# Kernel tuning notes

Hardware: AMD Instinct MI355X
Metric: run time of the kernel (lower is better)

The kernel has to match this reference:

```python
import jax, jax.numpy as jnp
import numpy as np

B, S, D, H = 128, 512, 256, 256


def _lstm_cell(Wih, Whh, b, x_t, h, c):
    # PyTorch LSTM gate order: i, f, g, o. b = b_ih + b_hh (mathematically equivalent).
    z = x_t @ Wih.T + h @ Whh.T + b  # [B, 4H]
    i, f, g, o = jnp.split(z, 4, axis=-1)
    i = jax.nn.sigmoid(i)
    f = jax.nn.sigmoid(f)
    g = jnp.tanh(g)
    o = jax.nn.sigmoid(o)
    c = f * c + i * g
    h = o * jnp.tanh(c)
    return h, c


def setup_inputs() -> dict:
    key = jax.random.key(0)
    ks = jax.random.split(key, 12)
    s = 1.0 / np.sqrt(H)
    f32 = jnp.float32
    return {
        "x": jax.random.normal(ks[0], (B, S, D), f32),
        "enc_Wih": jax.random.uniform(ks[1], (4 * H, D), f32, -s, s),
        "enc_Whh": jax.random.uniform(ks[2], (4 * H, H), f32, -s, s),
        "enc_b": jax.random.uniform(ks[3], (4 * H,), f32, -s, s),
        "dec_Wih": jax.random.uniform(ks[4], (4 * H, D), f32, -s, s),
        "dec_Whh": jax.random.uniform(ks[5], (4 * H, H), f32, -s, s),
        "dec_b": jax.random.uniform(ks[6], (4 * H,), f32, -s, s),
        "W1_w": jax.random.uniform(ks[7], (H, H), f32, -s, s),
        "W1_b": jax.random.uniform(ks[8], (H,), f32, -s, s),
        "W2_w": jax.random.uniform(ks[9], (H, H), f32, -s, s),
        "W2_b": jax.random.uniform(ks[10], (H,), f32, -s, s),
        "vt_w": jax.random.uniform(ks[11], (H,), f32, -s, s),
    }


def reference(x, enc_Wih, enc_Whh, enc_b, dec_Wih, dec_Whh, dec_b,
              W1_w, W1_b, W2_w, W2_b, vt_w):
    b_, s_, d_ = x.shape
    h0 = jnp.zeros((b_, H), x.dtype)
    c0 = jnp.zeros((b_, H), x.dtype)

    # ---- encoder LSTM over time ----
    def enc_step(carry, x_t):
        h, c = carry
        h, c = _lstm_cell(enc_Wih, enc_Whh, enc_b, x_t, h, c)
        return (h, c), h

    (h, c), enc_out = jax.lax.scan(enc_step, (h0, c0), jnp.swapaxes(x, 0, 1))
    enc_out = jnp.swapaxes(enc_out, 0, 1)  # [B, S, H]

    # W1(encoder_outputs) is loop-invariant; compute once (same math as original)
    enc_proj = enc_out @ W1_w.T + W1_b  # [B, S, H]

    # ---- pointer decode loop ----
    def dec_step(carry, _):
        h, c, din = carry
        h, c = _lstm_cell(dec_Wih, dec_Whh, dec_b, din, h, c)
        q = h @ W2_w.T + W2_b  # [B, H]
        u = jnp.einsum('bsh,h->bs', jnp.tanh(enc_proj + q[:, None, :]), vt_w)
        probs = jax.nn.softmax(u, axis=1)  # [B, S]
        din = jnp.einsum('bs,bsh->bh', probs, enc_out)
        return (h, c, din), probs

    din0 = jnp.zeros((b_, d_), x.dtype)
    _, probs_seq = jax.lax.scan(dec_step, (h, c, din0), None, length=s_)
    return jnp.swapaxes(probs_seq, 0, 1)  # [B, S, S]
```

## Files before the change

### kernel.cpp

```cpp
#include <hip/hip_runtime.h>
#include <hip/hip_fp16.h>

typedef _Float16 h2_t __attribute__((ext_vector_type(2)));
typedef unsigned int u32x4 __attribute__((ext_vector_type(4)));

#define KEXP 2.8853900817779268f

#define BARRIER() do { \
    asm volatile("s_waitcnt lgkmcnt(0)" ::: "memory"); \
    __builtin_amdgcn_s_barrier(); \
    asm volatile("" ::: "memory"); \
} while (0)

__device__ __forceinline__ float fdot2(unsigned int a, unsigned int b, float c) {
#if __has_builtin(__builtin_amdgcn_fdot2)
    return __builtin_amdgcn_fdot2(__builtin_bit_cast(h2_t, a), __builtin_bit_cast(h2_t, b), c, false);
#else
    h2_t ha = __builtin_bit_cast(h2_t, a), hb = __builtin_bit_cast(h2_t, b);
    return c + (float)ha[0]*(float)hb[0] + (float)ha[1]*(float)hb[1];
#endif
}

__device__ __forceinline__ unsigned int pk16(float a, float b) {
    auto h = __builtin_amdgcn_cvt_pkrtz(a, b);
    return __builtin_bit_cast(unsigned int, h);
}

__device__ __forceinline__ float rcp_(float x) {
#if __has_builtin(__builtin_amdgcn_rcpf)
    return __builtin_amdgcn_rcpf(x);
#else
    return 1.0f / x;
#endif
}

__device__ __forceinline__ float sigm(float x) { return rcp_(1.0f + __expf(-x)); }
__device__ __forceinline__ float tanh_(float x) {
    float e = __expf(2.0f * x);
    return 1.0f - 2.0f * rcp_(e + 1.0f);
}

__device__ __forceinline__ unsigned int rcp1p2exp(unsigned int s) {
    __half2 e = h2exp2(__builtin_bit_cast(__half2, s));
    __half2 d = __hadd2(e, __float2half2_rn(1.0f));
    return __builtin_bit_cast(unsigned int, h2rcp(d));
}
__device__ __forceinline__ unsigned int hadd2u(unsigned int a, unsigned int b) {
    return __builtin_bit_cast(unsigned int,
        __hadd2(__builtin_bit_cast(__half2, a), __builtin_bit_cast(__half2, b)));
}

__device__ __forceinline__ void st_u32(unsigned int* p, unsigned int v) {
    __hip_atomic_store(p, v, __ATOMIC_RELAXED, __HIP_MEMORY_SCOPE_AGENT);
}
__device__ __forceinline__ unsigned int ld_u32(const unsigned int* p) {
    return __hip_atomic_load(p, __ATOMIC_RELAXED, __HIP_MEMORY_SCOPE_AGENT);
}
__device__ __forceinline__ float h2f_lo(unsigned int v) {
    return __half2float(__ushort_as_half((unsigned short)(v & 0xffffu)));
}
__device__ __forceinline__ float h2f_hi(unsigned int v) {
    return __half2float(__ushort_as_half((unsigned short)(v >> 16)));
}

__device__ __forceinline__ void pair_sync(unsigned int* flags, int fo_me, int fo_pr,
                                          unsigned int target, int t) {
    BARRIER();
    if (t == 0) {
        st_u32(&flags[fo_me], target);
        while (ld_u32(&flags[fo_pr]) < target) __builtin_amdgcn_s_sleep(1);
    }
    BARRIER();
}

__global__ void init_flags_kernel(unsigned int* flags) {
    flags[threadIdx.x * 32] = 0u;
}

__global__ __launch_bounds__(256) void prep_kernel(
    const float* __restrict__ encWhh, const float* __restrict__ decWih,
    const float* __restrict__ decWhh, const float* __restrict__ W2w,
    u32x4* __restrict__ We8, u32x4* __restrict__ Wi8, u32x4* __restrict__ Wh8, u32x4* __restrict__ W28)
{
    int id = blockIdx.x * 256 + threadIdx.x;
    if (id < 3 * 32768) {
        int mat = id >> 15, local = id & 32767;
        int j = local & 1023, k8 = local >> 10;
        const float* src = mat == 0 ? encWhh : (mat == 1 ? decWih : decWhh);
        u32x4* dst = mat == 0 ? We8 : (mat == 1 ? Wi8 : Wh8);
        const float* p = src + (size_t)j * 256 + k8 * 8;
        float4 a = *(const float4*)p; float4 c = *(const float4*)(p + 4);
        u32x4 v; v[0] = pk16(a.x, a.y); v[1] = pk16(a.z, a.w);
        v[2] = pk16(c.x, c.y); v[3] = pk16(c.z, c.w);
        dst[k8 * 1024 + j] = v;
    } else {
        int local = id - 3 * 32768;
        if (local < 8192) {
            int m = local & 255, k8 = local >> 8;
            const float* p = W2w + (size_t)m * 256 + k8 * 8;
            float4 a = *(const float4*)p; float4 c = *(const float4*)(p + 4);
            u32x4 v; v[0] = pk16(a.x, a.y); v[1] = pk16(a.z, a.w);
            v[2] = pk16(c.x, c.y); v[3] = pk16(c.z, c.w);
            W28[k8 * 256 + m] = v;
        }
    }
}

template<int A_IS_F16, int TR_OUT>
__global__ __launch_bounds__(256) void gemm_kernel(
    const void* __restrict__ A_, const float* __restrict__ Bw,
    const float* __restrict__ bias, unsigned short* __restrict__ C, int N, float scale)
{
    __shared__ float As[16][68];
    __shared__ float Bs[16][132];
    const int t = threadIdx.x;
    const int row0 = blockIdx.y * 64, col0 = blockIdx.x * 128;
    const int ty = t >> 4, tx = t & 15;
    const int lm = t & 63, lkq = t >> 6;
    const int ln = t & 127, lkq2 = t >> 7;
    float acc[4][8] = {};
    for (int k0 = 0; k0 < 256; k0 += 16) {
        float4 av;
        if constexpr (A_IS_F16) {
            const unsigned short* A = (const unsigned short*)A_;
            uint2 ha = *(const uint2*)(A + (size_t)(row0 + lm) * 256 + k0 + lkq * 4);
            h2_t h0 = __builtin_bit_cast(h2_t, ha.x);
            h2_t h1 = __builtin_bit_cast(h2_t, ha.y);
            av = make_float4((float)h0[0], (float)h0[1], (float)h1[0], (float)h1[1]);
        } else {
            av = *(const float4*)((const float*)A_ + (size_t)(row0 + lm) * 256 + k0 + lkq * 4);
        }
        const float* bp = Bw + (size_t)(col0 + ln) * 256 + k0 + lkq2 * 8;
        float4 bv0 = *(const float4*)bp;
        float4 bv1 = *(const float4*)(bp + 4);
        __syncthreads();
        As[lkq * 4 + 0][lm] = av.x;
        As[lkq * 4 + 1][lm] = av.y;
        As[lkq * 4 + 2][lm] = av.z;
        As[lkq * 4 + 3][lm] = av.w;
        Bs[lkq2 * 8 + 0][ln] = bv0.x;
        Bs[lkq2 * 8 + 1][ln] = bv0.y;
        Bs[lkq2 * 8 + 2][ln] = bv0.z;
        Bs[lkq2 * 8 + 3][ln] = bv0.w;
        Bs[lkq2 * 8 + 4][ln] = bv1.x;
        Bs[lkq2 * 8 + 5][ln] = bv1.y;
        Bs[lkq2 * 8 + 6][ln] = bv1.z;
        Bs[lkq2 * 8 + 7][ln] = bv1.w;
        __syncthreads();
        #pragma unroll
        for (int kk = 0; kk < 16; ++kk) {
            float4 a = *(float4*)&As[kk][ty * 4];
            float4 b0 = *(float4*)&Bs[kk][tx * 8];
            float4 b1 = *(float4*)&Bs[kk][tx * 8 + 4];
            float ar[4] = {a.x, a.y, a.z, a.w};
            float br[8] = {b0.x, b0.y, b0.z, b0.w, b1.x, b1.y, b1.z, b1.w};
            #pragma unroll
            for (int i = 0; i < 4; ++i)
                #pragma unroll
                for (int j = 0; j < 8; ++j)
                    acc[i][j] = fmaf(ar[i], br[j], acc[i][j]);
        }
    }
    float bv[8];
    #pragma unroll
    for (int j = 0; j < 8; ++j) bv[j] = bias[col0 + tx * 8 + j];
    #pragma unroll
    for (int i = 0; i < 4; ++i) {
        unsigned int w0 = pk16((acc[i][0] + bv[0]) * scale, (acc[i][1] + bv[1]) * scale);
        unsigned int w1 = pk16((acc[i][2] + bv[2]) * scale, (acc[i][3] + bv[3]) * scale);
        unsigned int w2 = pk16((acc[i][4] + bv[4]) * scale, (acc[i][5] + bv[5]) * scale);
        unsigned int w3 = pk16((acc[i][6] + bv[6]) * scale, (acc[i][7] + bv[7]) * scale);
        uint4 val = make_uint4(w0, w1, w2, w3);
        if constexpr (TR_OUT) {
            int rr = row0 + ty * 4 + i;
            int bb = rr >> 9, s = rr & 511;
            int c8 = (col0 >> 3) + tx;
            ((uint4*)C)[(size_t)bb * 16384 + (size_t)c8 * 512 + s] = val;
        } else {
            *(uint4*)(C + (size_t)(row0 + ty * 4 + i) * N + col0 + tx * 8) = val;
        }
    }
}

__global__ __launch_bounds__(1024) void encoder_kernel(
    const unsigned short* __restrict__ Xproj, const u32x4* __restrict__ We8,
    float* __restrict__ hfin, float* __restrict__ cfin,
    unsigned short* __restrict__ enc_h, unsigned int* __restrict__ encT)
{
    const int b = blockIdx.x, t = threadIdx.x;
    __shared__ __align__(16) float zs[1024];
    __shared__ __align__(16) unsigned int hh2[128];
    if (t < 128) hh2[t] = 0u;
    float c_reg = 0.f, hprev = 0.f, hcur = 0.f;
    __syncthreads();
    const unsigned short* xp = Xproj + (size_t)b * 512 * 1024 + t;
    for (int step = 0; step < 512; ++step) {
        float acc = __half2float(__ushort_as_half(__builtin_nontemporal_load(xp)));
        #pragma unroll 8
        for (int k8 = 0; k8 < 32; ++k8) {
            u32x4 wv = We8[k8 * 1024 + t];
            u32x4 hv = *(const u32x4*)&hh2[k8 * 4];
            acc = fdot2(wv[0], hv[0], acc); acc = fdot2(wv[1], hv[1], acc);
            acc = fdot2(wv[2], hv[2], acc); acc = fdot2(wv[3], hv[3], acc);
        }
        zs[t] = acc;
        __syncthreads();
        if (t < 256) {
            float ig = sigm(zs[t]), fg = sigm(zs[t + 256]);
            float gg = tanh_(zs[t + 512]), og = sigm(zs[t + 768]);
            c_reg = fg * c_reg + ig * gg;
            float h = og * tanh_(c_reg);
            float hnb = __shfl_down(h, 1);
            if (!(t & 1)) hh2[t >> 1] = pk16(h, hnb);
            __builtin_nontemporal_store(__half_as_ushort(__float2half_rn(h)),
                                        enc_h + (size_t)(b * 512 + step) * 256 + t);
            if (step & 1) {
                int s2 = step >> 1;
                encT[(size_t)b * 65536 + (size_t)((s2 >> 2) * 256 + t) * 4 + (s2 & 3)] = pk16(hprev, h);
            }
            hprev = h; hcur = h;
        }
        __syncthreads();
        xp += 1024;
    }
    if (t < 256) { hfin[b * 256 + t] = hcur; cfin[b * 256 + t] = c_reg; }
}

__global__ __launch_bounds__(1024) void decoder_kernel(
    const u32x4* __restrict__ Wi8, const u32x4* __restrict__ Wh8, const u32x4* __restrict__ W28,
    const float* __restrict__ dec_b, const float* __restrict__ W2b, const float* __restrict__ vtw,
    const float* __restrict__ hfin, const float* __restrict__ cfin,
    const u32x4* __restrict__ projT, const u32x4* __restrict__ encT,
    unsigned int* __restrict__ xgate, unsigned int* __restrict__ xdin,
    unsigned int* __restrict__ xsum, unsigned int* __restrict__ flags,
    float* __restrict__ out)
{
    const int blk = blockIdx.x;
    const int b = blk & 127, r = blk >> 7;
    const int t = threadIdx.x;
    const int lane = t & 63, w = t >> 6;

    __shared__ __align__(16) float zs[1024];
    __shared__ __align__(16) unsigned int hh2[128];
    __shared__ __align__(16) unsigned int din2[128];
    __shared__ __align__(16) unsigned int qp2[128];
    __shared__ __align__(16) unsigned int mv2u[128];
    __shared__ __align__(16) unsigned int p2u[128];
    __shared__ float wreds[16];
    __shared__ float svtS, rsS;

    const int fo_me = (b * 2 + r) * 32, fo_pr = (b * 2 + (1 - r)) * 32;
    const int go_me = (b * 2 + r) * 256, go_pr = (b * 2 + (1 - r)) * 256;

    float c_reg = (t < 256) ? cfin[b * 256 + t] : 0.f;
    const float bja = (t < 256) ? dec_b[r * 512 + t] : 0.f;
    const float bjb = (t < 256) ? dec_b[r * 512 + 256 + t] : 0.f;
    const float w2b_r = (t < 256) ? W2b[t] : 0.f;
    if (t < 128) { din2[t] = 0u; mv2u[t] = pk16(-2.f * vtw[2 * t], -2.f * vtw[2 * t + 1]); }
    if (t < 256) zs[t] = vtw[t];
    __syncthreads();
    if (t < 64) {
        float v = zs[t] + zs[t + 64] + zs[t + 128] + zs[t + 192];
        #pragma unroll
        for (int off = 1; off < 64; off <<= 1) v += __shfl_xor(v, off);
        if (t == 0) svtS = v;
    }
    if (t < 256) {
        float h0 = hfin[b * 256 + t];
        float hnb = __shfl_down(h0, 1);
        if (!(t & 1)) hh2[t >> 1] = pk16(h0, hnb);
    }
    __syncthreads();
    const float svt = svtS;

    const int jl = t & 511, kh = t >> 9;
    const u32x4* wp = (kh ? Wh8 : Wi8) + (r * 512 + jl);
    const unsigned int* vls = kh ? (const unsigned int*)hh2 : (const unsigned int*)din2;
    const int hF = t & 255, slF = t >> 8;
    const int sl4 = t >> 2, qr = t & 3;
    const int s_g = r * 256 + sl4;
    const u32x4* pD = projT + (size_t)b * 16384 + (size_t)(qr * 8) * 512 + s_g;
    const u32x4* fD = encT + (size_t)b * 16384 + (size_t)(r * 32 + slF * 8) * 256 + hF;
    float* outp = out + (size_t)b * 262144;

    for (int step = 0; step < 512; ++step) {
        float acc = 0.f;
        #pragma unroll 8
        for (int k8 = 0; k8 < 32; ++k8) {
            u32x4 wv = wp[k8 * 1024];
            u32x4 hv = *(const u32x4*)&vls[k8 * 4];
            acc = fdot2(wv[0], hv[0], acc); acc = fdot2(wv[1], hv[1], acc);
            acc = fdot2(wv[2], hv[2], acc); acc = fdot2(wv[3], hv[3], acc);
        }
        zs[t] = acc;
        BARRIER();
        unsigned int myg = 0u;
        if (t < 256) {
            float z_a = bja + zs[t] + zs[t + 512];
            float z_b = bjb + zs[t + 256] + zs[t + 768];
            float ga, gb;
            if (r == 0) { ga = sigm(z_a); gb = sigm(z_b); }
            else        { ga = tanh_(z_a); gb = sigm(z_b); }
            myg = (unsigned int)__half_as_ushort(__float2half_rn(ga)) |
                  ((unsigned int)__half_as_ushort(__float2half_rn(gb)) << 16);
            st_u32(&xgate[go_me + t], myg);
            asm volatile("s_waitcnt vmcnt(0)" ::: "memory");
        }
        pair_sync(flags, fo_me, fo_pr, (unsigned)(3 * step + 1), t);
        if (t < 256) {
            unsigned int og = ld_u32(&xgate[go_pr + t]);
            float la = h2f_lo(myg), lb = h2f_hi(myg);
            float oa = h2f_lo(og),  ob = h2f_hi(og);
            float gi, gf, gg, go_;
            if (r == 0) { gi = la; gf = lb; gg = oa; go_ = ob; }
            else        { gg = la; go_ = lb; gi = oa; gf = ob; }
            c_reg = gf * c_reg + gi * gg;
            float h = go_ * tanh_(c_reg);
            float hnb = __shfl_down(h, 1);
            if (!(t & 1)) hh2[t >> 1] = pk16(h, hnb);
        }
        BARRIER();
        {
            float qa = 0.f;
            #pragma unroll
            for (int i = 0; i < 8; ++i) {
                int k8 = slF * 8 + i;
                u32x4 wv = W28[k8 * 256 + hF];
                u32x4 hv = *(const u32x4*)&hh2[k8 * 4];
                qa = fdot2(wv[0], hv[0], qa); qa = fdot2(wv[1], hv[1], qa);
                qa = fdot2(wv[2], hv[2], qa); qa = fdot2(wv[3], hv[3], qa);
            }
            zs[t] = qa;
        }
        BARRIER();
        if (t < 256) {
            float q = (w2b_r + zs[t] + zs[t + 256] + zs[t + 512] + zs[t + 768]) * KEXP;
            float qnx = __shfl_down(q, 1);
            if (!(t & 1)) qp2[t >> 1] = pk16(q, qnx);
        }
        BARRIER();
        float e;
        u32x4 fv[8];
        {
            float up = 0.f;
            #pragma unroll 4
            for (int i = 0; i < 8; ++i) {
                u32x4 pv = pD[i * 512];
                int c = qr * 8 + i;
                u32x4 qh = *(const u32x4*)&qp2[c * 4];
                u32x4 mv = *(const u32x4*)&mv2u[c * 4];
                up = fdot2(mv[0], rcp1p2exp(hadd2u(pv[0], qh[0])), up);
                up = fdot2(mv[1], rcp1p2exp(hadd2u(pv[1], qh[1])), up);
                up = fdot2(mv[2], rcp1p2exp(hadd2u(pv[2], qh[2])), up);
                up = fdot2(mv[3], rcp1p2exp(hadd2u(pv[3], qh[3])), up);
            }
            up += __shfl_xor(up, 1);
            up += __shfl_xor(up, 2);
            e = __expf(up + svt);
            #pragma unroll
            for (int j = 0; j < 8; ++j) fv[j] = fD[j * 256];
            float ws = e;
            #pragma unroll
            for (int off = 1; off < 64; off <<= 1) ws += __shfl_xor(ws, off);
            if (lane == 0) wreds[w] = ws;
        }
        BARRIER();
        if (t == 0) {
            float ls = 0.f;
            #pragma unroll
            for (int k = 0; k < 16; ++k) ls += wreds[k];
            ls *= 0.25f;
            st_u32(&xsum[fo_me], __builtin_bit_cast(unsigned int, ls));
            asm volatile("s_waitcnt vmcnt(0)" ::: "memory");
            st_u32(&flags[fo_me], (unsigned)(3 * step + 2));
            while (ld_u32(&flags[fo_pr]) < (unsigned)(3 * step + 2)) __builtin_amdgcn_s_sleep(1);
            float lr = __builtin_bit_cast(float, ld_u32(&xsum[fo_pr]));
            rsS = rcp_(ls + lr);
        }
        BARRIER();
        {
            float rs = rsS;
            float p = e * rs;
            if ((t & 3) == 0) outp[(size_t)step * 512 + s_g] = p;
            float pnx = __shfl_down(p, 4);
            if ((t & 7) == 0) p2u[t >> 3] = pk16(p, pnx);
        }
        BARRIER();
        {
            float fa = 0.f;
            #pragma unroll
            for (int j = 0; j < 8; ++j) {
                u32x4 ev = fv[j];
                int base = (slF * 8 + j) * 4;
                u32x4 pw = *(const u32x4*)&p2u[base];
                fa = fdot2(ev[0], pw[0], fa); fa = fdot2(ev[1], pw[1], fa);
                fa = fdot2(ev[2], pw[2], fa); fa = fdot2(ev[3], pw[3], fa);
            }
            zs[t] = fa;
        }
        BARRIER();
        float dpart = 0.f;
        if (t < 256) {
            dpart = zs[t] + zs[t + 256] + zs[t + 512] + zs[t + 768];
            st_u32(&xdin[go_me + t], __builtin_bit_cast(unsigned int, dpart));
            asm volatile("s_waitcnt vmcnt(0)" ::: "memory");
        }
        pair_sync(flags, fo_me, fo_pr, (unsigned)(3 * step + 3), t);
        if (t < 256) {
            float drem = __builtin_bit_cast(float, ld_u32(&xdin[go_pr + t]));
            float dval = dpart + drem;
            float dnx = __shfl_down(dval, 1);
            if (!(t & 1)) din2[t >> 1] = pk16(dval, dnx);
        }
        BARRIER();
    }
}

extern "C" void kernel_launch(void* const* d_in, const int* in_sizes, int n_in,
                              void* d_out, int out_size, void* d_ws, size_t ws_size,
                              hipStream_t stream) {
    const float* x      = (const float*)d_in[0];
    const float* encWih = (const float*)d_in[1];
    const float* encWhh = (const float*)d_in[2];
    const float* enc_b  = (const float*)d_in[3];
    const float* decWih = (const float*)d_in[4];
    const float* decWhh = (const float*)d_in[5];
    const float* dec_bp = (const float*)d_in[6];
    const float* W1w    = (const float*)d_in[7];
    const float* W1b    = (const float*)d_in[8];
    const float* W2w    = (const float*)d_in[9];
    const float* W2bp   = (const float*)d_in[10];
    const float* vtw    = (const float*)d_in[11];

    char* ws = (char*)d_ws;
    u32x4* We8 = (u32x4*)(ws);
    u32x4* Wi8 = (u32x4*)(ws + 524288);
    u32x4* Wh8 = (u32x4*)(ws + 1048576);
    u32x4* W28 = (u32x4*)(ws + 1572864);
    unsigned short* enc_h = (unsigned short*)(ws + 1703936);
    unsigned int*   encT  = (unsigned int*)(ws + 35258368);
    unsigned short* projT = (unsigned short*)(ws + 68812800);
    float* hfin = (float*)(ws + 102367232);
    float* cfin = (float*)(ws + 102498304);

    unsigned int* flags = (unsigned int*)(ws + 1703936);
    unsigned int* xsum  = (unsigned int*)(ws + 1703936 + 32768);
    unsigned int* xgate = (unsigned int*)(ws + 1703936 + 65536);
    unsigned int* xdin  = (unsigned int*)(ws + 1703936 + 65536 + 262144);

    unsigned short* Xproj = (unsigned short*)d_out;

    prep_kernel<<<416, 256, 0, stream>>>(encWhh, decWih, decWhh, W2w, We8, Wi8, Wh8, W28);
    gemm_kernel<0, 0><<<dim3(8, 1024), 256, 0, stream>>>(x, encWih, enc_b, Xproj, 1024, 1.0f);
    encoder_kernel<<<128, 1024, 0, stream>>>(Xproj, We8, hfin, cfin, enc_h, (unsigned int*)encT);
    gemm_kernel<1, 1><<<dim3(2, 1024), 256, 0, stream>>>(enc_h, W1w, W1b, projT, 256, KEXP);
    init_flags_kernel<<<1, 256, 0, stream>>>(flags);
    decoder_kernel<<<256, 1024, 0, stream>>>(Wi8, Wh8, W28, dec_bp, W2bp, vtw,
                                             hfin, cfin, (const u32x4*)projT, (const u32x4*)encT,
                                             xgate, xdin, xsum, flags, (float*)d_out);
}
```

Before: 14.14 ms.

## Split decoder per batch across four 512-thread blocks with merged sync points

Measured after the change: 16.86 ms. +19.2%, slower.

```diff
diff --git a/kernel.cpp b/kernel.cpp
--- a/kernel.cpp
+++ b/kernel.cpp
@@ -61,16 +61,6 @@
 }
 __device__ __forceinline__ float h2f_hi(unsigned int v) {
     return __half2float(__ushort_as_half((unsigned short)(v >> 16)));
-}
-
-__device__ __forceinline__ void pair_sync(unsigned int* flags, int fo_me, int fo_pr,
-                                          unsigned int target, int t) {
-    BARRIER();
-    if (t == 0) {
-        st_u32(&flags[fo_me], target);
-        while (ld_u32(&flags[fo_pr]) < target) __builtin_amdgcn_s_sleep(1);
-    }
-    BARRIER();
 }
 
 __global__ void init_flags_kernel(unsigned int* flags) {
@@ -226,7 +216,7 @@
     if (t < 256) { hfin[b * 256 + t] = hcur; cfin[b * 256 + t] = c_reg; }
 }
 
-__global__ __launch_bounds__(1024) void decoder_kernel(
+__global__ __launch_bounds__(512, 4) void decoder_kernel(
     const u32x4* __restrict__ Wi8, const u32x4* __restrict__ Wh8, const u32x4* __restrict__ W28,
     const float* __restrict__ dec_b, const float* __restrict__ W2b, const float* __restrict__ vtw,
     const float* __restrict__ hfin, const float* __restrict__ cfin,
@@ -236,27 +226,36 @@
     float* __restrict__ out)
 {
     const int blk = blockIdx.x;
-    const int b = blk & 127, r = blk >> 7;
+    const int b = blk & 127, g = blk >> 7;
     const int t = threadIdx.x;
     const int lane = t & 63, w = t >> 6;
 
-    __shared__ __align__(16) float zs[1024];
+    __shared__ __align__(16) float zs[512];
     __shared__ __align__(16) unsigned int hh2[128];
     __shared__ __align__(16) unsigned int din2[128];
     __shared__ __align__(16) unsigned int qp2[128];
     __shared__ __align__(16) unsigned int mv2u[128];
-    __shared__ __align__(16) unsigned int p2u[128];
-    __shared__ float wreds[16];
+    __shared__ __align__(16) unsigned int p2u[64];
+    __shared__ float wreds[8];
     __shared__ float svtS, rsS;
 
-    const int fo_me = (b * 2 + r) * 32, fo_pr = (b * 2 + (1 - r)) * 32;
-    const int go_me = (b * 2 + r) * 256, go_pr = (b * 2 + (1 - r)) * 256;
-
-    float c_reg = (t < 256) ? cfin[b * 256 + t] : 0.f;
-    const float bja = (t < 256) ? dec_b[r * 512 + t] : 0.f;
-    const float bjb = (t < 256) ? dec_b[r * 512 + 256 + t] : 0.f;
+    const int q4 = b * 4 + g;
+    unsigned int* fl_me = flags + q4 * 32;
+    unsigned int* fl_p0 = flags + (b * 4 + ((g + 1) & 3)) * 32;
+    unsigned int* fl_p1 = flags + (b * 4 + ((g + 2) & 3)) * 32;
+    unsigned int* fl_p2 = flags + (b * 4 + ((g + 3) & 3)) * 32;
+    unsigned int* xg_me = xgate + q4 * 128;
+    unsigned int* xd_me = xdin + q4 * 256;
+
+    float ca = 0.f, cb = 0.f;
+    if (t < 128) {
+        ca = cfin[b * 256 + 2 * t];
+        cb = cfin[b * 256 + 2 * t + 1];
+        din2[t] = 0u;
+        mv2u[t] = pk16(-2.f * vtw[2 * t], -2.f * vtw[2 * t + 1]);
+    }
+    const float bja = (t < 256) ? dec_b[g * 256 + t] : 0.f;
     const float w2b_r = (t < 256) ? W2b[t] : 0.f;
-    if (t < 128) { din2[t] = 0u; mv2u[t] = pk16(-2.f * vtw[2 * t], -2.f * vtw[2 * t + 1]); }
     if (t < 256) zs[t] = vtw[t];
     __syncthreads();
     if (t < 64) {
@@ -273,14 +272,14 @@
     __syncthreads();
     const float svt = svtS;
 
-    const int jl = t & 511, kh = t >> 9;
-    const u32x4* wp = (kh ? Wh8 : Wi8) + (r * 512 + jl);
+    const int jl = t & 255, kh = t >> 8;
+    const u32x4* wp = (kh ? Wh8 : Wi8) + (g * 256 + jl);
     const unsigned int* vls = kh ? (const unsigned int*)hh2 : (const unsigned int*)din2;
-    const int hF = t & 255, slF = t >> 8;
+    const int mC = t & 255, sc = t >> 8;
     const int sl4 = t >> 2, qr = t & 3;
-    const int s_g = r * 256 + sl4;
+    const int s_g = g * 128 + sl4;
     const u32x4* pD = projT + (size_t)b * 16384 + (size_t)(qr * 8) * 512 + s_g;
-    const u32x4* fD = encT + (size_t)b * 16384 + (size_t)(r * 32 + slF * 8) * 256 + hF;
+    const u32x4* fD = encT + (size_t)b * 16384 + (size_t)(g * 16 + sc * 8) * 256 + mC;
     float* outp = out + (size_t)b * 262144;
 
     for (int step = 0; step < 512; ++step) {
@@ -294,38 +293,45 @@
         }
         zs[t] = acc;
         BARRIER();
-        unsigned int myg = 0u;
         if (t < 256) {
-            float z_a = bja + zs[t] + zs[t + 512];
-            float z_b = bjb + zs[t + 256] + zs[t + 768];
-            float ga, gb;
-            if (r == 0) { ga = sigm(z_a); gb = sigm(z_b); }
-            else        { ga = tanh_(z_a); gb = sigm(z_b); }
-            myg = (unsigned int)__half_as_ushort(__float2half_rn(ga)) |
-                  ((unsigned int)__half_as_ushort(__float2half_rn(gb)) << 16);
-            st_u32(&xgate[go_me + t], myg);
-            asm volatile("s_waitcnt vmcnt(0)" ::: "memory");
-        }
-        pair_sync(flags, fo_me, fo_pr, (unsigned)(3 * step + 1), t);
-        if (t < 256) {
-            unsigned int og = ld_u32(&xgate[go_pr + t]);
-            float la = h2f_lo(myg), lb = h2f_hi(myg);
-            float oa = h2f_lo(og),  ob = h2f_hi(og);
-            float gi, gf, gg, go_;
-            if (r == 0) { gi = la; gf = lb; gg = oa; go_ = ob; }
-            else        { gg = la; go_ = lb; gi = oa; gf = ob; }
-            c_reg = gf * c_reg + gi * gg;
-            float h = go_ * tanh_(c_reg);
-            float hnb = __shfl_down(h, 1);
-            if (!(t & 1)) hh2[t >> 1] = pk16(h, hnb);
+            float z = bja + zs[t] + zs[t + 256];
+            float gv = (g == 2) ? tanh_(z) : sigm(z);
+            float gnx = __shfl_down(gv, 1);
+            if (!(t & 1))
+                st_u32(&xg_me[t >> 1],
+                       (unsigned int)__half_as_ushort(__float2half_rn(gv)) |
+                       ((unsigned int)__half_as_ushort(__float2half_rn(gnx)) << 16));
+        }
+        asm volatile("s_waitcnt vmcnt(0)" ::: "memory");
+        BARRIER();
+        if (t == 0) {
+            unsigned int T = (unsigned)(2 * step + 1);
+            st_u32(fl_me, T);
+            for (;;) {
+                unsigned int f0 = ld_u32(fl_p0), f1 = ld_u32(fl_p1), f2 = ld_u32(fl_p2);
+                if (f0 >= T && f1 >= T && f2 >= T) break;
+                __builtin_amdgcn_s_sleep(1);
+            }
+        }
+        BARRIER();
+        if (t < 128) {
+            unsigned int G0 = ld_u32(&xgate[(b * 4 + 0) * 128 + t]);
+            unsigned int G1 = ld_u32(&xgate[(b * 4 + 1) * 128 + t]);
+            unsigned int G2 = ld_u32(&xgate[(b * 4 + 2) * 128 + t]);
+            unsigned int G3 = ld_u32(&xgate[(b * 4 + 3) * 128 + t]);
+            ca = h2f_lo(G1) * ca + h2f_lo(G0) * h2f_lo(G2);
+            cb = h2f_hi(G1) * cb + h2f_hi(G0) * h2f_hi(G2);
+            float ha = h2f_lo(G3) * tanh_(ca);
+            float hb = h2f_hi(G3) * tanh_(cb);
+            hh2[t] = pk16(ha, hb);
         }
         BARRIER();
         {
             float qa = 0.f;
             #pragma unroll
-            for (int i = 0; i < 8; ++i) {
-                int k8 = slF * 8 + i;
-                u32x4 wv = W28[k8 * 256 + hF];
+            for (int i = 0; i < 16; ++i) {
+                int k8 = sc * 16 + i;
+                u32x4 wv = W28[k8 * 256 + mC];
                 u32x4 hv = *(const u32x4*)&hh2[k8 * 4];
                 qa = fdot2(wv[0], hv[0], qa); qa = fdot2(wv[1], hv[1], qa);
                 qa = fdot2(wv[2], hv[2], qa); qa = fdot2(wv[3], hv[3], qa);
@@ -334,7 +340,7 @@
         }
         BARRIER();
         if (t < 256) {
-            float q = (w2b_r + zs[t] + zs[t + 256] + zs[t + 512] + zs[t + 768]) * KEXP;
+            float q = (w2b_r + zs[t] + zs[t + 256]) * KEXP;
             float qnx = __shfl_down(q, 1);
             if (!(t & 1)) qp2[t >> 1] = pk16(q, qnx);
         }
@@ -359,58 +365,69 @@
             e = __expf(up + svt);
             #pragma unroll
             for (int j = 0; j < 8; ++j) fv[j] = fD[j * 256];
+            float enx = __shfl_down(e, 4);
+            if (!(t & 7)) p2u[t >> 3] = pk16(e, enx);
             float ws = e;
             #pragma unroll
             for (int off = 1; off < 64; off <<= 1) ws += __shfl_xor(ws, off);
             if (lane == 0) wreds[w] = ws;
         }
         BARRIER();
+        {
+            float fa = 0.f;
+            #pragma unroll
+            for (int j = 0; j < 8; ++j) {
+                u32x4 ev = fv[j];
+                u32x4 pw = *(const u32x4*)&p2u[(sc * 8 + j) * 4];
+                fa = fdot2(ev[0], pw[0], fa); fa = fdot2(ev[1], pw[1], fa);
+                fa = fdot2(ev[2], pw[2], fa); fa = fdot2(ev[3], pw[3], fa);
+            }
+            zs[t] = fa;
+        }
+        BARRIER();
+        float dpart = 0.f;
+        if (t < 256) {
+            dpart = zs[t] + zs[t + 256];
+            st_u32(&xd_me[t], __builtin_bit_cast(unsigned int, dpart));
+        }
         if (t == 0) {
             float ls = 0.f;
             #pragma unroll
-            for (int k = 0; k < 16; ++k) ls += wreds[k];
-            ls *= 0.25f;
-            st_u32(&xsum[fo_me], __builtin_bit_cast(unsigned int, ls));
-            asm volatile("s_waitcnt vmcnt(0)" ::: "memory");
-            st_u32(&flags[fo_me], (unsigned)(3 * step + 2));
-            while (ld_u32(&flags[fo_pr]) < (unsigned)(3 * step + 2)) __builtin_amdgcn_s_sleep(1);
-            float lr = __builtin_bit_cast(float, ld_u32(&xsum[fo_pr]));
-            rsS = rcp_(ls + lr);
+            for (int k = 0; k < 8; ++k) ls += wreds[k];
+            st_u32(&xsum[q4 * 32], __builtin_bit_cast(unsigned int, ls * 0.25f));
+        }
+        asm volatile("s_waitcnt vmcnt(0)" ::: "memory");
+        BARRIER();
+        if (t == 0) {
+            unsigned int T = (unsigned)(2 * step + 2);
+            st_u32(fl_me, T);
+            for (;;) {
+                unsigned int f0 = ld_u32(fl_p0), f1 = ld_u32(fl_p1), f2 = ld_u32(fl_p2);
+                if (f0 >= T && f1 >= T && f2 >= T) break;
+                __builtin_amdgcn_s_sleep(1);
+            }
+            float gs = __builtin_bit_cast(float, ld_u32(&xsum[(b * 4 + 0) * 32]))
+                     + __builtin_bit_cast(float, ld_u32(&xsum[(b * 4 + 1) * 32]))
+                     + __builtin_bit_cast(float, ld_u32(&xsum[(b * 4 + 2) * 32]))
+                     + __builtin_bit_cast(float, ld_u32(&xsum[(b * 4 + 3) * 32]));
+            rsS = rcp_(gs);
         }
         BARRIER();
         {
             float rs = rsS;
-            float p = e * rs;
-            if ((t & 3) == 0) outp[(size_t)step * 512 + s_g] = p;
-            float pnx = __shfl_down(p, 4);
-            if ((t & 7) == 0) p2u[t >> 3] = pk16(p, pnx);
-        }
-        BARRIER();
-        {
-            float fa = 0.f;
-            #pragma unroll
-            for (int j = 0; j < 8; ++j) {
-                u32x4 ev = fv[j];
-                int base = (slF * 8 + j) * 4;
-                u32x4 pw = *(const u32x4*)&p2u[base];
-                fa = fdot2(ev[0], pw[0], fa); fa = fdot2(ev[1], pw[1], fa);
-                fa = fdot2(ev[2], pw[2], fa); fa = fdot2(ev[3], pw[3], fa);
-            }
-            zs[t] = fa;
-        }
-        BARRIER();
-        float dpart = 0.f;
-        if (t < 256) {
-            dpart = zs[t] + zs[t + 256] + zs[t + 512] + zs[t + 768];
-            st_u32(&xdin[go_me + t], __builtin_bit_cast(unsigned int, dpart));
-            asm volatile("s_waitcnt vmcnt(0)" ::: "memory");
-        }
-        pair_sync(flags, fo_me, fo_pr, (unsigned)(3 * step + 3), t);
-        if (t < 256) {
-            float drem = __builtin_bit_cast(float, ld_u32(&xdin[go_pr + t]));
-            float dval = dpart + drem;
-            float dnx = __shfl_down(dval, 1);
-            if (!(t & 1)) din2[t >> 1] = pk16(dval, dnx);
+            if (t < 256) {
+                float dsum = dpart;
+                #pragma unroll
+                for (int dg = 1; dg < 4; ++dg) {
+                    int gp = (g + dg) & 3;
+                    dsum += __builtin_bit_cast(float, ld_u32(&xdin[(b * 4 + gp) * 256 + t]));
+                }
+                float dval = dsum * rs;
+                float dnx = __shfl_down(dval, 1);
+                if (!(t & 1)) din2[t >> 1] = pk16(dval, dnx);
+            }
+            if ((t & 3) == 0)
+                outp[(size_t)step * 512 + s_g] = e * rs;
         }
         BARRIER();
     }
@@ -444,9 +461,9 @@
     float* cfin = (float*)(ws + 102498304);
 
     unsigned int* flags = (unsigned int*)(ws + 1703936);
-    unsigned int* xsum  = (unsigned int*)(ws + 1703936 + 32768);
-    unsigned int* xgate = (unsigned int*)(ws + 1703936 + 65536);
-    unsigned int* xdin  = (unsigned int*)(ws + 1703936 + 65536 + 262144);
+    unsigned int* xsum  = (unsigned int*)(ws + 1703936 + 65536);
+    unsigned int* xgate = (unsigned int*)(ws + 1703936 + 131072);
+    unsigned int* xdin  = (unsigned int*)(ws + 1703936 + 131072 + 262144);
 
     unsigned short* Xproj = (unsigned short*)d_out;
 
@@ -454,8 +471,8 @@
     gemm_kernel<0, 0><<<dim3(8, 1024), 256, 0, stream>>>(x, encWih, enc_b, Xproj, 1024, 1.0f);
     encoder_kernel<<<128, 1024, 0, stream>>>(Xproj, We8, hfin, cfin, enc_h, (unsigned int*)encT);
     gemm_kernel<1, 1><<<dim3(2, 1024), 256, 0, stream>>>(enc_h, W1w, W1b, projT, 256, KEXP);
-    init_flags_kernel<<<1, 256, 0, stream>>>(flags);
-    decoder_kernel<<<256, 1024, 0, stream>>>(Wi8, Wh8, W28, dec_bp, W2bp, vtw,
-                                             hfin, cfin, (const u32x4*)projT, (const u32x4*)encT,
-                                             xgate, xdin, xsum, flags, (float*)d_out);
-}
+    init_flags_kernel<<<1, 512, 0, stream>>>(flags);
+    decoder_kernel<<<512, 512, 0, stream>>>(Wi8, Wh8, W28, dec_bp, W2bp, vtw,
+                                            hfin, cfin, (const u32x4*)projT, (const u32x4*)encT,
+                                            xgate, xdin, xsum, flags, (float*)d_out);
+}
```

## Defer softmax normalization to merge two cross-block syncs per decode step

Applied to the files above, without the earlier changes.

New measurement: 16.13 ms. 14.1% more time.

```diff
diff --git a/kernel.cpp b/kernel.cpp
--- a/kernel.cpp
+++ b/kernel.cpp
@@ -21,6 +21,12 @@
 #endif
 }
 
+__device__ __forceinline__ float dot4(u32x4 a, u32x4 b, float c) {
+    c = fdot2(a[0], b[0], c); c = fdot2(a[1], b[1], c);
+    c = fdot2(a[2], b[2], c); c = fdot2(a[3], b[3], c);
+    return c;
+}
+
 __device__ __forceinline__ unsigned int pk16(float a, float b) {
     auto h = __builtin_amdgcn_cvt_pkrtz(a, b);
     return __builtin_bit_cast(unsigned int, h);
@@ -56,21 +62,14 @@
 __device__ __forceinline__ unsigned int ld_u32(const unsigned int* p) {
     return __hip_atomic_load(p, __ATOMIC_RELAXED, __HIP_MEMORY_SCOPE_AGENT);
 }
+__device__ __forceinline__ float ld_f32(const unsigned int* p) {
+    return __builtin_bit_cast(float, ld_u32(p));
+}
 __device__ __forceinline__ float h2f_lo(unsigned int v) {
     return __half2float(__ushort_as_half((unsigned short)(v & 0xffffu)));
 }
 __device__ __forceinline__ float h2f_hi(unsigned int v) {
     return __half2float(__ushort_as_half((unsigned short)(v >> 16)));
-}
-
-__device__ __forceinline__ void pair_sync(unsigned int* flags, int fo_me, int fo_pr,
-                                          unsigned int target, int t) {
-    BARRIER();
-    if (t == 0) {
-        st_u32(&flags[fo_me], target);
-        while (ld_u32(&flags[fo_pr]) < target) __builtin_amdgcn_s_sleep(1);
-    }
-    BARRIER();
 }
 
 __global__ void init_flags_kernel(unsigned int* flags) {
@@ -200,8 +199,7 @@
         for (int k8 = 0; k8 < 32; ++k8) {
             u32x4 wv = We8[k8 * 1024 + t];
             u32x4 hv = *(const u32x4*)&hh2[k8 * 4];
-            acc = fdot2(wv[0], hv[0], acc); acc = fdot2(wv[1], hv[1], acc);
-            acc = fdot2(wv[2], hv[2], acc); acc = fdot2(wv[3], hv[3], acc);
+            acc = dot4(wv, hv, acc);
         }
         zs[t] = acc;
         __syncthreads();
@@ -249,13 +247,16 @@
     __shared__ float wreds[16];
     __shared__ float svtS, rsS;
 
-    const int fo_me = (b * 2 + r) * 32, fo_pr = (b * 2 + (1 - r)) * 32;
-    const int go_me = (b * 2 + r) * 256, go_pr = (b * 2 + (1 - r)) * 256;
-
-    float c_reg = (t < 256) ? cfin[b * 256 + t] : 0.f;
+    const int pr_me = b * 2 + r, pr_pa = b * 2 + (1 - r);
+    unsigned int* fl_me = flags + pr_me * 32;
+    unsigned int* fl_pa = flags + pr_pa * 32;
+    unsigned int* xg_me = xgate + pr_me * 256;
+    unsigned int* xd_me = xdin + pr_me * 256;
+
     const float bja = (t < 256) ? dec_b[r * 512 + t] : 0.f;
     const float bjb = (t < 256) ? dec_b[r * 512 + 256 + t] : 0.f;
     const float w2b_r = (t < 256) ? W2b[t] : 0.f;
+    float c_reg = (t < 256) ? cfin[b * 256 + t] : 0.f;
     if (t < 128) { din2[t] = 0u; mv2u[t] = pk16(-2.f * vtw[2 * t], -2.f * vtw[2 * t + 1]); }
     if (t < 256) zs[t] = vtw[t];
     __syncthreads();
@@ -276,11 +277,10 @@
     const int jl = t & 511, kh = t >> 9;
     const u32x4* wp = (kh ? Wh8 : Wi8) + (r * 512 + jl);
     const unsigned int* vls = kh ? (const unsigned int*)hh2 : (const unsigned int*)din2;
-    const int hF = t & 255, slF = t >> 8;
-    const int sl4 = t >> 2, qr = t & 3;
-    const int s_g = r * 256 + sl4;
-    const u32x4* pD = projT + (size_t)b * 16384 + (size_t)(qr * 8) * 512 + s_g;
-    const u32x4* fD = encT + (size_t)b * 16384 + (size_t)(r * 32 + slF * 8) * 256 + hF;
+    const int hC = t & 255, slC = t >> 8;
+    const int sq = t >> 2, qr = t & 3;
+    const u32x4* pD = projT + (size_t)b * 16384 + (size_t)(qr * 8) * 512 + r * 256 + sq;
+    const u32x4* fD = encT + (size_t)b * 16384 + (size_t)(r * 32 + slC * 8) * 256 + hC;
     float* outp = out + (size_t)b * 262144;
 
     for (int step = 0; step < 512; ++step) {
@@ -289,8 +289,7 @@
         for (int k8 = 0; k8 < 32; ++k8) {
             u32x4 wv = wp[k8 * 1024];
             u32x4 hv = *(const u32x4*)&vls[k8 * 4];
-            acc = fdot2(wv[0], hv[0], acc); acc = fdot2(wv[1], hv[1], acc);
-            acc = fdot2(wv[2], hv[2], acc); acc = fdot2(wv[3], hv[3], acc);
+            acc = dot4(wv, hv, acc);
         }
         zs[t] = acc;
         BARRIER();
@@ -303,12 +302,21 @@
             else        { ga = tanh_(z_a); gb = sigm(z_b); }
             myg = (unsigned int)__half_as_ushort(__float2half_rn(ga)) |
                   ((unsigned int)__half_as_ushort(__float2half_rn(gb)) << 16);
-            st_u32(&xgate[go_me + t], myg);
+            st_u32(&xg_me[t], myg);
             asm volatile("s_waitcnt vmcnt(0)" ::: "memory");
         }
-        pair_sync(flags, fo_me, fo_pr, (unsigned)(3 * step + 1), t);
+        BARRIER();
+        if (t == 0) {
+            unsigned int T = (unsigned)(2 * step + 1);
+            st_u32(fl_me, T);
+            while (ld_u32(fl_pa) < T) __builtin_amdgcn_s_sleep(1);
+        }
+        BARRIER();
+        u32x4 pv[8];
+        #pragma unroll
+        for (int i = 0; i < 8; ++i) pv[i] = pD[i * 512];
         if (t < 256) {
-            unsigned int og = ld_u32(&xgate[go_pr + t]);
+            unsigned int og = ld_u32(&xgate[pr_pa * 256 + t]);
             float la = h2f_lo(myg), lb = h2f_hi(myg);
             float oa = h2f_lo(og),  ob = h2f_hi(og);
             float gi, gf, gg, go_;
@@ -324,11 +332,10 @@
             float qa = 0.f;
             #pragma unroll
             for (int i = 0; i < 8; ++i) {
-                int k8 = slF * 8 + i;
-                u32x4 wv = W28[k8 * 256 + hF];
+                int k8 = slC * 8 + i;
+                u32x4 wv = W28[k8 * 256 + hC];
                 u32x4 hv = *(const u32x4*)&hh2[k8 * 4];
-                qa = fdot2(wv[0], hv[0], qa); qa = fdot2(wv[1], hv[1], qa);
-                qa = fdot2(wv[2], hv[2], qa); qa = fdot2(wv[3], hv[3], qa);
+                qa = dot4(wv, hv, qa);
             }
             zs[t] = qa;
         }
@@ -342,59 +349,36 @@
         float e;
         u32x4 fv[8];
         {
-            float up = 0.f;
-            #pragma unroll 4
+            float u = 0.f;
+            #pragma unroll
             for (int i = 0; i < 8; ++i) {
-                u32x4 pv = pD[i * 512];
                 int c = qr * 8 + i;
                 u32x4 qh = *(const u32x4*)&qp2[c * 4];
                 u32x4 mv = *(const u32x4*)&mv2u[c * 4];
-                up = fdot2(mv[0], rcp1p2exp(hadd2u(pv[0], qh[0])), up);
-                up = fdot2(mv[1], rcp1p2exp(hadd2u(pv[1], qh[1])), up);
-                up = fdot2(mv[2], rcp1p2exp(hadd2u(pv[2], qh[2])), up);
-                up = fdot2(mv[3], rcp1p2exp(hadd2u(pv[3], qh[3])), up);
+                u = fdot2(mv[0], rcp1p2exp(hadd2u(pv[i][0], qh[0])), u);
+                u = fdot2(mv[1], rcp1p2exp(hadd2u(pv[i][1], qh[1])), u);
+                u = fdot2(mv[2], rcp1p2exp(hadd2u(pv[i][2], qh[2])), u);
+                u = fdot2(mv[3], rcp1p2exp(hadd2u(pv[i][3], qh[3])), u);
             }
-            up += __shfl_xor(up, 1);
-            up += __shfl_xor(up, 2);
-            e = __expf(up + svt);
+            u += __shfl_xor(u, 1);
+            u += __shfl_xor(u, 2);
+            e = __expf(u + svt);
             #pragma unroll
             for (int j = 0; j < 8; ++j) fv[j] = fD[j * 256];
+            float enx = __shfl_down(e, 4);
+            if (!(t & 7)) p2u[t >> 3] = pk16(e, enx);
             float ws = e;
             #pragma unroll
             for (int off = 1; off < 64; off <<= 1) ws += __shfl_xor(ws, off);
             if (lane == 0) wreds[w] = ws;
         }
         BARRIER();
-        if (t == 0) {
-            float ls = 0.f;
-            #pragma unroll
-            for (int k = 0; k < 16; ++k) ls += wreds[k];
-            ls *= 0.25f;
-            st_u32(&xsum[fo_me], __builtin_bit_cast(unsigned int, ls));
-            asm volatile("s_waitcnt vmcnt(0)" ::: "memory");
-            st_u32(&flags[fo_me], (unsigned)(3 * step + 2));
-            while (ld_u32(&flags[fo_pr]) < (unsigned)(3 * step + 2)) __builtin_amdgcn_s_sleep(1);
-            float lr = __builtin_bit_cast(float, ld_u32(&xsum[fo_pr]));
-            rsS = rcp_(ls + lr);
-        }
-        BARRIER();
-        {
-            float rs = rsS;
-            float p = e * rs;
-            if ((t & 3) == 0) outp[(size_t)step * 512 + s_g] = p;
-            float pnx = __shfl_down(p, 4);
-            if ((t & 7) == 0) p2u[t >> 3] = pk16(p, pnx);
-        }
-        BARRIER();
         {
             float fa = 0.f;
             #pragma unroll
             for (int j = 0; j < 8; ++j) {
-                u32x4 ev = fv[j];
-                int base = (slF * 8 + j) * 4;
-                u32x4 pw = *(const u32x4*)&p2u[base];
-                fa = fdot2(ev[0], pw[0], fa); fa = fdot2(ev[1], pw[1], fa);
-                fa = fdot2(ev[2], pw[2], fa); fa = fdot2(ev[3], pw[3], fa);
+                u32x4 pw = *(const u32x4*)&p2u[(slC * 8 + j) * 4];
+                fa = dot4(fv[j], pw, fa);
             }
             zs[t] = fa;
         }
@@ -402,15 +386,36 @@
         float dpart = 0.f;
         if (t < 256) {
             dpart = zs[t] + zs[t + 256] + zs[t + 512] + zs[t + 768];
-            st_u32(&xdin[go_me + t], __builtin_bit_cast(unsigned int, dpart));
-            asm volatile("s_waitcnt vmcnt(0)" ::: "memory");
-        }
-        pair_sync(flags, fo_me, fo_pr, (unsigned)(3 * step + 3), t);
-        if (t < 256) {
-            float drem = __builtin_bit_cast(float, ld_u32(&xdin[go_pr + t]));
-            float dval = dpart + drem;
-            float dnx = __shfl_down(dval, 1);
-            if (!(t & 1)) din2[t >> 1] = pk16(dval, dnx);
+            st_u32(&xd_me[t], __builtin_bit_cast(unsigned int, dpart));
+        }
+        if (t == 0) {
+            float ls = 0.f;
+            #pragma unroll
+            for (int k = 0; k < 16; ++k) ls += wreds[k];
+            st_u32(&xsum[pr_me * 32], __builtin_bit_cast(unsigned int, ls * 0.25f));
+        }
+        asm volatile("s_waitcnt vmcnt(0)" ::: "memory");
+        BARRIER();
+        if (t == 0) {
+            unsigned int T = (unsigned)(2 * step + 2);
+            st_u32(fl_me, T);
+            while (ld_u32(fl_pa) < T) __builtin_amdgcn_s_sleep(1);
+            float ls = 0.f;
+            #pragma unroll
+            for (int k = 0; k < 16; ++k) ls += wreds[k];
+            float gs = ls * 0.25f + ld_f32(&xsum[pr_pa * 32]);
+            rsS = rcp_(gs);
+        }
+        BARRIER();
+        {
+            float rs = rsS;
+            if (t < 256) {
+                float dval = (dpart + ld_f32(&xdin[pr_pa * 256 + t])) * rs;
+                float dnx = __shfl_down(dval, 1);
+                if (!(t & 1)) din2[t >> 1] = pk16(dval, dnx);
+            }
+            if (!(t & 3))
+                outp[(size_t)step * 512 + r * 256 + sq] = e * rs;
         }
         BARRIER();
     }
```

## Defer softmax normalization to merge cross-block sum and din exchanges

Applied to the files above, without the earlier changes.

New measurement: 13.86 ms. -2.0%, faster.

```diff
diff --git a/kernel.cpp b/kernel.cpp
--- a/kernel.cpp
+++ b/kernel.cpp
@@ -21,6 +21,12 @@
 #endif
 }
 
+__device__ __forceinline__ float dot4(u32x4 a, u32x4 b, float c) {
+    c = fdot2(a[0], b[0], c); c = fdot2(a[1], b[1], c);
+    c = fdot2(a[2], b[2], c); c = fdot2(a[3], b[3], c);
+    return c;
+}
+
 __device__ __forceinline__ unsigned int pk16(float a, float b) {
     auto h = __builtin_amdgcn_cvt_pkrtz(a, b);
     return __builtin_bit_cast(unsigned int, h);
@@ -56,21 +62,14 @@
 __device__ __forceinline__ unsigned int ld_u32(const unsigned int* p) {
     return __hip_atomic_load(p, __ATOMIC_RELAXED, __HIP_MEMORY_SCOPE_AGENT);
 }
+__device__ __forceinline__ float ld_f32(const unsigned int* p) {
+    return __builtin_bit_cast(float, ld_u32(p));
+}
 __device__ __forceinline__ float h2f_lo(unsigned int v) {
     return __half2float(__ushort_as_half((unsigned short)(v & 0xffffu)));
 }
 __device__ __forceinline__ float h2f_hi(unsigned int v) {
     return __half2float(__ushort_as_half((unsigned short)(v >> 16)));
-}
-
-__device__ __forceinline__ void pair_sync(unsigned int* flags, int fo_me, int fo_pr,
-                                          unsigned int target, int t) {
-    BARRIER();
-    if (t == 0) {
-        st_u32(&flags[fo_me], target);
-        while (ld_u32(&flags[fo_pr]) < target) __builtin_amdgcn_s_sleep(1);
-    }
-    BARRIER();
 }
 
 __global__ void init_flags_kernel(unsigned int* flags) {
@@ -200,8 +199,7 @@
         for (int k8 = 0; k8 < 32; ++k8) {
             u32x4 wv = We8[k8 * 1024 + t];
             u32x4 hv = *(const u32x4*)&hh2[k8 * 4];
-            acc = fdot2(wv[0], hv[0], acc); acc = fdot2(wv[1], hv[1], acc);
-            acc = fdot2(wv[2], hv[2], acc); acc = fdot2(wv[3], hv[3], acc);
+            acc = dot4(wv, hv, acc);
         }
         zs[t] = acc;
         __syncthreads();
@@ -289,8 +287,7 @@
         for (int k8 = 0; k8 < 32; ++k8) {
             u32x4 wv = wp[k8 * 1024];
             u32x4 hv = *(const u32x4*)&vls[k8 * 4];
-            acc = fdot2(wv[0], hv[0], acc); acc = fdot2(wv[1], hv[1], acc);
-            acc = fdot2(wv[2], hv[2], acc); acc = fdot2(wv[3], hv[3], acc);
+            acc = dot4(wv, hv, acc);
         }
         zs[t] = acc;
         BARRIER();
@@ -306,7 +303,13 @@
             st_u32(&xgate[go_me + t], myg);
             asm volatile("s_waitcnt vmcnt(0)" ::: "memory");
         }
-        pair_sync(flags, fo_me, fo_pr, (unsigned)(3 * step + 1), t);
+        BARRIER();
+        if (t == 0) {
+            unsigned int T = (unsigned)(2 * step + 1);
+            st_u32(&flags[fo_me], T);
+            while (ld_u32(&flags[fo_pr]) < T) __builtin_amdgcn_s_sleep(1);
+        }
+        BARRIER();
         if (t < 256) {
             unsigned int og = ld_u32(&xgate[go_pr + t]);
             float la = h2f_lo(myg), lb = h2f_hi(myg);
@@ -327,8 +330,7 @@
                 int k8 = slF * 8 + i;
                 u32x4 wv = W28[k8 * 256 + hF];
                 u32x4 hv = *(const u32x4*)&hh2[k8 * 4];
-                qa = fdot2(wv[0], hv[0], qa); qa = fdot2(wv[1], hv[1], qa);
-                qa = fdot2(wv[2], hv[2], qa); qa = fdot2(wv[3], hv[3], qa);
+                qa = dot4(wv, hv, qa);
             }
             zs[t] = qa;
         }
@@ -359,42 +361,21 @@
             e = __expf(up + svt);
             #pragma unroll
             for (int j = 0; j < 8; ++j) fv[j] = fD[j * 256];
+            float enx = __shfl_down(e, 4);
+            if (!(t & 7)) p2u[t >> 3] = pk16(e, enx);
             float ws = e;
             #pragma unroll
             for (int off = 1; off < 64; off <<= 1) ws += __shfl_xor(ws, off);
             if (lane == 0) wreds[w] = ws;
         }
         BARRIER();
-        if (t == 0) {
-            float ls = 0.f;
-            #pragma unroll
-            for (int k = 0; k < 16; ++k) ls += wreds[k];
-            ls *= 0.25f;
-            st_u32(&xsum[fo_me], __builtin_bit_cast(unsigned int, ls));
-            asm volatile("s_waitcnt vmcnt(0)" ::: "memory");
-            st_u32(&flags[fo_me], (unsigned)(3 * step + 2));
-            while (ld_u32(&flags[fo_pr]) < (unsigned)(3 * step + 2)) __builtin_amdgcn_s_sleep(1);
-            float lr = __builtin_bit_cast(float, ld_u32(&xsum[fo_pr]));
-            rsS = rcp_(ls + lr);
-        }
-        BARRIER();
-        {
-            float rs = rsS;
-            float p = e * rs;
-            if ((t & 3) == 0) outp[(size_t)step * 512 + s_g] = p;
-            float pnx = __shfl_down(p, 4);
-            if ((t & 7) == 0) p2u[t >> 3] = pk16(p, pnx);
-        }
-        BARRIER();
         {
             float fa = 0.f;
             #pragma unroll
             for (int j = 0; j < 8; ++j) {
                 u32x4 ev = fv[j];
-                int base = (slF * 8 + j) * 4;
-                u32x4 pw = *(const u32x4*)&p2u[base];
-                fa = fdot2(ev[0], pw[0], fa); fa = fdot2(ev[1], pw[1], fa);
-                fa = fdot2(ev[2], pw[2], fa); fa = fdot2(ev[3], pw[3], fa);
+                u32x4 pw = *(const u32x4*)&p2u[(slF * 8 + j) * 4];
+                fa = dot4(ev, pw, fa);
             }
             zs[t] = fa;
         }
@@ -405,12 +386,30 @@
             st_u32(&xdin[go_me + t], __builtin_bit_cast(unsigned int, dpart));
             asm volatile("s_waitcnt vmcnt(0)" ::: "memory");
         }
-        pair_sync(flags, fo_me, fo_pr, (unsigned)(3 * step + 3), t);
-        if (t < 256) {
-            float drem = __builtin_bit_cast(float, ld_u32(&xdin[go_pr + t]));
-            float dval = dpart + drem;
-            float dnx = __shfl_down(dval, 1);
-            if (!(t & 1)) din2[t >> 1] = pk16(dval, dnx);
+        BARRIER();
+        if (t == 0) {
+            float ls = 0.f;
+            #pragma unroll
+            for (int k = 0; k < 16; ++k) ls += wreds[k];
+            ls *= 0.25f;
+            st_u32(&xsum[fo_me], __builtin_bit_cast(unsigned int, ls));
+            asm volatile("s_waitcnt vmcnt(0)" ::: "memory");
+            unsigned int T = (unsigned)(2 * step + 2);
+            st_u32(&flags[fo_me], T);
+            while (ld_u32(&flags[fo_pr]) < T) __builtin_amdgcn_s_sleep(1);
+            float lr = __builtin_bit_cast(float, ld_u32(&xsum[fo_pr]));
+            rsS = rcp_(ls + lr);
+        }
+        BARRIER();
+        {
+            float rs = rsS;
+            if (t < 256) {
+                float drem = __builtin_bit_cast(float, ld_u32(&xdin[go_pr + t]));
+                float dval = (dpart + drem) * rs;
+                float dnx = __shfl_down(dval, 1);
+                if (!(t & 1)) din2[t >> 1] = pk16(dval, dnx);
+            }
+            if ((t & 3) == 0) outp[(size_t)step * 512 + s_g] = e * rs;
         }
         BARRIER();
     }
```
